# Kernel optimization log

Measured on AMD Instinct MI355X. Metric: run time of the kernel, lower is better.

## Reference

```python
import jax, jax.numpy as jnp
import numpy as np
from jax import lax

DEPTH = 2
HEADS = 8
TEMP = 1.0

def _ln_last(x, g, b, eps=1e-5):
    m = x.mean(-1, keepdims=True)
    v = ((x - m) ** 2).mean(-1, keepdims=True)
    return (x - m) / jnp.sqrt(v + eps) * g + b

def _ln_chan(x, g, b, eps=1e-6):
    # torch custom LayerNorm over channel dim of NCHW, biased var
    m = x.mean(1, keepdims=True)
    v = ((x - m) ** 2).mean(1, keepdims=True)
    return (x - m) / jnp.sqrt(v + eps) * g[None, :, None, None] + b[None, :, None, None]

def _conv3x3(x, w):
    return lax.conv_general_dilated(x, w, (1, 1), ((1, 1), (1, 1)),
                                    dimension_numbers=('NCHW', 'OIHW', 'NCHW'))

def _transformer(x, ln1_g, ln1_b, qkv_w, qkv_b, out_w, out_b, ln2_g, ln2_b,
                 mlp_w1, mlp_b1, mlp_w2, mlp_b2):
    dim = x.shape[-1]
    dh = dim // HEADS
    scale = dh ** -0.5
    for i in range(DEPTH):
        h = _ln_last(x, ln1_g[i], ln1_b[i])
        qkv = h @ qkv_w[i] + qkv_b[i]
        q, k, v = jnp.split(qkv, 3, axis=-1)
        sp = lambda t: t.reshape(t.shape[0], t.shape[1], HEADS, dh).transpose(0, 2, 1, 3)
        q, k, v = sp(q), sp(k), sp(v)
        attn = jax.nn.softmax(jnp.einsum('bhid,bhjd->bhij', q, k) * scale, axis=-1) / TEMP
        o = jnp.einsum('bhij,bhjd->bhid', attn, v).transpose(0, 2, 1, 3).reshape(x.shape)
        x = o @ out_w[i] + out_b[i] + x
        h = _ln_last(x, ln2_g[i], ln2_b[i])
        x = jax.nn.gelu(h @ mlp_w1[i] + mlp_b1[i], approximate=False) @ mlp_w2[i] + mlp_b2[i] + x
    return x

def _tacf(support_feature, query_feature, task_descriptor, ln1_g, ln1_b, qkv_w, qkv_b,
          out_w, out_b, ln2_g, ln2_b, mlp_w1, mlp_b1, mlp_w2, mlp_b2,
          rfm_ln_g, rfm_ln_b, rfm_conv1, rfm_conv2, rfm_conv3, rfm_conv4):
    n, c, h, w = support_feature.shape
    M = task_descriptor.shape[1]
    # descriptor generator: 'n c h w -> 1 (n h w) c', prepend descriptors
    sf = support_feature.transpose(0, 2, 3, 1).reshape(1, n * h * w, c)
    x = jnp.concatenate([task_descriptor, sf], axis=1)
    x = _transformer(x, ln1_g, ln1_b, qkv_w, qkv_b, out_w, out_b, ln2_g, ln2_b,
                     mlp_w1, mlp_b1, mlp_w2, mlp_b2)
    key0 = x[0, :M, :]  # (M, C)

    def region(feat):
        # mean over C of feat[:,None,c,h,w]*key[m,c] == matmul / C
        return jax.nn.sigmoid(jnp.einsum('bchw,mc->bmhw', feat, key0) / feat.shape[1])

    def map_fuse(reg, feat):
        # mean over m of (feat*task + feat) == feat*(mean_m(task)+1)
        return feat * (reg.mean(1, keepdims=True) + 1.0)

    def rfm(x4):
        t = _ln_chan(x4, rfm_ln_g, rfm_ln_b)
        t = jax.nn.relu(_conv3x3(t, rfm_conv1))
        t = jax.nn.relu(_conv3x3(t, rfm_conv2))
        t = jax.nn.relu(_conv3x3(t, rfm_conv3))
        t = _conv3x3(t, rfm_conv4)
        b_, T_, h_, w_ = t.shape
        t = jax.nn.sigmoid(t.reshape(b_, T_, h_ * w_))  # (B,T,HW)
        feat = x4.transpose(0, 2, 3, 1).reshape(b_, h_ * w_, -1)  # (B,HW,C)
        out = jnp.einsum('btp,bpc->btc', t, feat) / (h_ * w_)  # mean over HW
        return out.transpose(0, 2, 1)  # (B,C,T)

    qr = region(query_feature)
    sr = region(support_feature)
    aq = map_fuse(qr, query_feature)
    asp = map_fuse(sr, support_feature)
    return (rfm(asp), rfm(aq))

def setup_inputs() -> dict:
    key = jax.random.key(0)
    ks = jax.random.split(key, 12)
    B_S, B_Q, C, H, W = 25, 75, 128, 10, 10
    M, T, MLP = 16, 32, 512
    rn = lambda k, s, sc=1.0: jax.random.normal(k, s, dtype=jnp.float32) * sc
    return {
        'support_feature': rn(ks[0], (B_S, C, H, W)),
        'query_feature': rn(ks[1], (B_Q, C, H, W)),
        'task_descriptor': rn(ks[2], (1, M, C)),
        'ln1_g': jnp.ones((DEPTH, C), jnp.float32), 'ln1_b': jnp.zeros((DEPTH, C), jnp.float32),
        'qkv_w': rn(ks[3], (DEPTH, C, 3 * C), 0.02), 'qkv_b': jnp.zeros((DEPTH, 3 * C), jnp.float32),
        'out_w': rn(ks[4], (DEPTH, C, C), 0.02), 'out_b': jnp.zeros((DEPTH, C), jnp.float32),
        'ln2_g': jnp.ones((DEPTH, C), jnp.float32), 'ln2_b': jnp.zeros((DEPTH, C), jnp.float32),
        'mlp_w1': rn(ks[5], (DEPTH, C, MLP), 0.02), 'mlp_b1': jnp.zeros((DEPTH, MLP), jnp.float32),
        'mlp_w2': rn(ks[6], (DEPTH, MLP, C), 0.02), 'mlp_b2': jnp.zeros((DEPTH, C), jnp.float32),
        'rfm_ln_g': jnp.ones((C,), jnp.float32), 'rfm_ln_b': jnp.zeros((C,), jnp.float32),
        'rfm_conv1': rn(ks[7], (T, C, 3, 3), 0.05),
        'rfm_conv2': rn(ks[8], (T, T, 3, 3), 0.05),
        'rfm_conv3': rn(ks[9], (T, T, 3, 3), 0.05),
        'rfm_conv4': rn(ks[10], (T, T, 3, 3), 0.05),
    }

def reference(support_feature, query_feature, task_descriptor, ln1_g, ln1_b, qkv_w, qkv_b,
              out_w, out_b, ln2_g, ln2_b, mlp_w1, mlp_b1, mlp_w2, mlp_b2,
              rfm_ln_g, rfm_ln_b, rfm_conv1, rfm_conv2, rfm_conv3, rfm_conv4):
    return _tacf(support_feature, query_feature, task_descriptor, ln1_g, ln1_b, qkv_w, qkv_b,
                 out_w, out_b, ln2_g, ln2_b, mlp_w1, mlp_b1, mlp_w2, mlp_b2,
                 rfm_ln_g, rfm_ln_b, rfm_conv1, rfm_conv2, rfm_conv3, rfm_conv4)
```

## Files before the change

### kernel.cpp

```cpp
#include <hip/hip_runtime.h>
#include <math.h>

#define SEQ 2516
#define SEQP 2520
#define SEQP2 2560
#define CDIM 128

typedef __attribute__((ext_vector_type(8))) short short8;
typedef __attribute__((ext_vector_type(4))) float f32x4;

__device__ __forceinline__ float gelu_exact(float x) {
    return x * 0.5f * (1.0f + erff(x * 0.7071067811865475f));
}
__device__ __forceinline__ float fexp2(float x) { return __builtin_amdgcn_exp2f(x); }
__device__ __forceinline__ short f2bf(float f) {
    unsigned u = __float_as_uint(f);
    unsigned r = 0x7fffu + ((u >> 16) & 1u);
    return (short)((u + r) >> 16);
}
__device__ __forceinline__ short f2bf_trunc(float f) {
    return (short)(__float_as_uint(f) >> 16);
}

__global__ __launch_bounds__(64) void concat_ln_kernel(
// ... 199 lines not shown
    const int grp = __builtin_amdgcn_readfirstlane(t >> 7);
    const int r0 = blockIdx.x * 8 + grp * 2;
    float acc0 = 0.f, acc1 = 0.f;
    #pragma unroll
    for (int h = 0; h < 8; ++h) {
        const float* p0a = PART + ((size_t)h * SEQP + r0) * 20;
        const float* p1a = PART + ((size_t)(8 + h) * SEQP + r0) * 20;
        const float* p0b = p0a + 20;
        const float* p1b = p1a + 20;
        float m0 = p0a[16], l0 = p0a[17], m1 = p1a[16], l1 = p1a[17];
        float Ma = fmaxf(m0, m1);
        float w0 = fexp2(m0 - Ma), w1 = fexp2(m1 - Ma);
        float inva = 1.f / fmaf(l0, w0, l1 * w1);
        float c0a = w0 * inva, c1a = w1 * inva;
        m0 = p0b[16]; l0 = p0b[17]; m1 = p1b[16]; l1 = p1b[17];
        float Mb = fmaxf(m0, m1);
        w0 = fexp2(m0 - Mb); w1 = fexp2(m1 - Mb);
        float invb = 1.f / fmaf(l0, w0, l1 * w1);
        float c0b = w0 * invb, c1b = w1 * invb;
        #pragma unroll
        for (int kk = 0; kk < 4; ++kk) {
            const int k0 = h * 16 + kk * 4;
            float w_0 = W[(size_t)(k0 + 0) * 128 + c];
            float w_1 = W[(size_t)(k0 + 1) * 128 + c];
            float w_2 = W[(size_t)(k0 + 2) * 128 + c];
            float w_3 = W[(size_t)(k0 + 3) * 128 + c];
            float4 x0 = *(const float4*)&p0a[kk * 4];
            float4 y0 = *(const float4*)&p1a[kk * 4];
            float4 x1 = *(const float4*)&p0b[kk * 4];
            float4 y1 = *(const float4*)&p1b[kk * 4];
            float a00 = x0.x * c0a + y0.x * c1a;
            float a01 = x0.y * c0a + y0.y * c1a;
            float a02 = x0.z * c0a + y0.z * c1a;
            float a03 = x0.w * c0a + y0.w * c1a;
            float a10 = x1.x * c0b + y1.x * c1b;
            float a11 = x1.y * c0b + y1.y * c1b;
            float a12 = x1.z * c0b + y1.z * c1b;
            float a13 = x1.w * c0b + y1.w * c1b;
            acc0 = fmaf(a00, w_0, acc0); acc0 = fmaf(a01, w_1, acc0);
            acc0 = fmaf(a02, w_2, acc0); acc0 = fmaf(a03, w_3, acc0);
            acc1 = fmaf(a10, w_0, acc1); acc1 = fmaf(a11, w_1, acc1);
            acc1 = fmaf(a12, w_2, acc1); acc1 = fmaf(a13, w_3, acc1);
        }
    }
    float bv = bias[c];
    float v0 = acc0 + bv + R[(size_t)(r0 + 0) * 128 + c];
    float v1 = acc1 + bv + R[(size_t)(r0 + 1) * 128 + c];
    ln[grp * 2 + 0][c] = v0;
    ln[grp * 2 + 1][c] = v1;
    if (r0 + 0 < M) C[(size_t)(r0 + 0) * 128 + c] = v0;
    if (r0 + 1 < M) C[(size_t)(r0 + 1) * 128 + c] = v1;
    __syncthreads();
    const int wv = t >> 6, l = t & 63;
    float x0 = ln[wv][l], x1 = ln[wv][l + 64];
    float s = x0 + x1;
    for (int off = 32; off > 0; off >>= 1) s += __shfl_down(s, off);
    float mean = __shfl(s, 0) * (1.f / 128.f);
    float d0 = x0 - mean, d1 = x1 - mean;
    float vv = d0 * d0 + d1 * d1;
    for (int off = 32; off > 0; off >>= 1) vv += __shfl_down(vv, off);
    float var = __shfl(vv, 0) * (1.f / 128.f);
    float rstd = rsqrtf(var + 1e-5f);
    const int hrow = blockIdx.x * 8 + wv;
    H[(size_t)hrow * 128 + l]      = d0 * rstd * g[l] + bb[l];
    H[(size_t)hrow * 128 + 64 + l] = d1 * rstd * g[l + 64] + bb[l + 64];
}

__global__ __launch_bounds__(256) void mlp_fused_kernel(
    const float* __restrict__ A, const float* __restrict__ W1,
    const float* __restrict__ b1, const float* __restrict__ W2,
    float* __restrict__ PARTG) {
    __shared__ __align__(16) short W1t[64 * 136];
    __shared__ __align__(16) short W2t[128 * 72];
    __shared__ __align__(16) short Ct[4 * 16 * 72];
    const int t = threadIdx.x;
    const int wave = t >> 6, lane = t & 63;
    const int quad = lane >> 4, c16 = lane & 15;
    const int m0 = blockIdx.x * 64;
    const int kz = blockIdx.y;
    const int n0 = kz * 64;
    #pragma unroll
    for (int pass = 0; pass < 4; ++pass) {
        int idx = t + pass * 256;
        int n = idx & 63, kc = idx >> 6;
        short8 wv;
        #pragma unroll
        for (int j = 0; j < 8; ++j)
            wv[j] = f2bf(W1[(size_t)(kc * 8 + j) * 512 + n0 + n]);
        *(short8*)&W1t[n * 136 + kc * 8] = wv;
    }
    {
        const int n = t & 127, half = t >> 7;
        #pragma unroll
        for (int c = 0; c < 4; ++c) {
            short8 wv;
            #pragma unroll
            for (int j = 0; j < 8; ++j)
                wv[j] = f2bf(W2[(size_t)(n0 + half * 32 + c * 8 + j) * 128 + n]);
            *(short8*)&W2t[n * 72 + half * 32 + c * 8] = wv;
        }
    }
    __syncthreads();
    const int am = m0 + wave * 16 + c16;
    f32x4 acc1[4];
    #pragma unroll
    for (int i = 0; i < 4; ++i) acc1[i] = (f32x4){0.f, 0.f, 0.f, 0.f};
    #pragma unroll
    for (int kk = 0; kk < 4; ++kk) {
        const float4* ap = (const float4*)(A + (size_t)am * 128 + kk * 32 + quad * 8);
        float4 a0 = ap[0], a1 = ap[1];
        short8 af;
        af[0] = f2bf(a0.x); af[1] = f2bf(a0.y); af[2] = f2bf(a0.z); af[3] = f2bf(a0.w);
        af[4] = f2bf(a1.x); af[5] = f2bf(a1.y); af[6] = f2bf(a1.z); af[7] = f2bf(a1.w);
        #pragma unroll
        for (int ns = 0; ns < 4; ++ns) {
            short8 wf = *(const short8*)&W1t[(ns * 16 + c16) * 136 + kk * 32 + quad * 8];
            acc1[ns] = __builtin_amdgcn_mfma_f32_16x16x32_bf16(af, wf, acc1[ns], 0, 0, 0);
        }
    }
    short* Cw = Ct + wave * 16 * 72;
    #pragma unroll
    for (int ns = 0; ns < 4; ++ns) {
        float bv = b1[n0 + ns * 16 + c16];
        #pragma unroll
        for (int r = 0; r < 4; ++r)
            Cw[(quad * 4 + r) * 72 + ns * 16 + c16] = f2bf(gelu_exact(acc1[ns][r] + bv));
    }
    f32x4 acc2[8];
    #pragma unroll
    for (int i = 0; i < 8; ++i) acc2[i] = (f32x4){0.f, 0.f, 0.f, 0.f};
    #pragma unroll
    for (int kk = 0; kk < 2; ++kk) {
        short8 af2 = *(const short8*)&Cw[c16 * 72 + kk * 32 + quad * 8];
        #pragma unroll
        for (int ns = 0; ns < 8; ++ns) {
            short8 wf = *(const short8*)&W2t[(ns * 16 + c16) * 72 + kk * 32 + quad * 8];
            acc2[ns] = __builtin_amdgcn_mfma_f32_16x16x32_bf16(af2, wf, acc2[ns], 0, 0, 0);
        }
    }
    float* dst = PARTG + (size_t)kz * SEQP2 * 128;
    #pragma unroll
    for (int ns = 0; ns < 8; ++ns) {
        #pragma unroll
        for (int r = 0; r < 4; ++r) {
            const int row = m0 + wave * 16 + quad * 4 + r;
            dst[(size_t)row * 128 + ns * 16 + c16] = acc2[ns][r];
        }
    }
}

__global__ __launch_bounds__(512) void combine_ln_kernel(
    const float* __restrict__ PARTG, const float* __restrict__ bias,
    const float* __restrict__ R, float* __restrict__ C, float* __restrict__ H,
    const float* __restrict__ g, const float* __restrict__ bb, int M) {
    __shared__ float ln[8][130];
    const int t = threadIdx.x;
    const int c = t & 127;
    const int grp = __builtin_amdgcn_readfirstlane(t >> 7);
    const int r0 = blockIdx.x * 8 + grp * 2;
    #pragma unroll
    for (int i = 0; i < 2; ++i) {
        const int row = r0 + i;
        float v = bias[c] + R[(size_t)row * 128 + c];
        #pragma unroll
        for (int kz = 0; kz < 8; ++kz)
            v += PARTG[(size_t)kz * SEQP2 * 128 + (size_t)row * 128 + c];
        ln[grp * 2 + i][c] = v;
        if (row < M) C[(size_t)row * 128 + c] = v;
    }
    __syncthreads();
    const int wv = t >> 6, l = t & 63;
    float x0 = ln[wv][l], x1 = ln[wv][l + 64];
    float s = x0 + x1;
    for (int off = 32; off > 0; off >>= 1) s += __shfl_down(s, off);
    float mean = __shfl(s, 0) * (1.f / 128.f);
    float d0 = x0 - mean, d1 = x1 - mean;
    float vv = d0 * d0 + d1 * d1;
    for (int off = 32; off > 0; off >>= 1) vv += __shfl_down(vv, off);
    float var = __shfl(vv, 0) * (1.f / 128.f);
    float rstd = rsqrtf(var + 1e-5f);
    const int hrow = blockIdx.x * 8 + wv;
    H[(size_t)hrow * 128 + l]      = d0 * rstd * g[l] + bb[l];
    H[(size_t)hrow * 128 + 64 + l] = d1 * rstd * g[l + 64] + bb[l + 64];
}

__global__ __launch_bounds__(256) void region_fuse_stats_kernel(
    const float* __restrict__ sup, const float* __restrict__ qry,
    const float* __restrict__ X, float* __restrict__ FUSEDT,
    float* __restrict__ MEAN, float* __restrict__ RSTD) {
    __shared__ float key0[2048];
    __shared__ float rfac[100];
    const int b = blockIdx.x;
    const int t = threadIdx.x;
    const float* feat = (b < 25) ? (sup + (size_t)b * 12800) : (qry + (size_t)(b - 25) * 12800);
    for (int i = t; i < 2048; i += 256) key0[i] = X[i];
    __syncthreads();
    if (t < 100) {
        float dots[16];
        #pragma unroll
        for (int mm = 0; mm < 16; ++mm) dots[mm] = 0.f;
        float s = 0.f, ss = 0.f;
        for (int c = 0; c < 128; ++c) {
            float f = feat[c * 100 + t];
            s += f; ss += f * f;
            #pragma unroll
            for (int mm = 0; mm < 16; ++mm) dots[mm] += f * key0[mm * 128 + c];
        }
        float mean16 = 0.f;
        #pragma unroll
        for (int mm = 0; mm < 16; ++mm) mean16 += 1.f / (1.f + expf(-dots[mm] * (1.f / 128.f)));
        float r = mean16 * (1.f / 16.f) + 1.f;
        rfac[t] = r;
        float mr = s * (1.f / 128.f);
        float vr = ss * (1.f / 128.f) - mr * mr;
        MEAN[b * 128 + t] = mr * r;
        RSTD[b * 128 + t] = rsqrtf(vr * r * r + 1e-6f);
    }
    __syncthreads();
    for (int i = t; i < 12800; i += 256) {
        int p = i >> 7, c = i & 127;
        FUSEDT[(size_t)b * 12800 + i] = feat[c * 100 + p] * rfac[p];
    }
}

__global__ __launch_bounds__(256) void conv1_mfma_kernel(
    const float* __restrict__ FUSEDT, const float* __restrict__ MEAN,
    const float* __restrict__ RSTD, const float* __restrict__ g,
    const float* __restrict__ bb, const float* __restrict__ w,
    short* __restrict__ C1) {
    __shared__ __align__(16) short inT[144 * 136];
    __shared__ __align__(16) short Wt[32 * 136];
    const int b = blockIdx.x;
    const int t = threadIdx.x;
    const int wave = t >> 6, lane = t & 63;
    const int quad = lane >> 4, c16 = lane & 15;
    for (int idx = t; idx < 2304; idx += 256) {
        int pos = idx >> 4, cg = idx & 15;
        int yy = pos / 12, xx = pos - yy * 12;
        short8 sv;
        if (yy >= 1 && yy <= 10 && xx >= 1 && xx <= 10) {
            int pp = (yy - 1) * 10 + (xx - 1);
            const float4* fp = (const float4*)(FUSEDT + (size_t)b * 12800 + pp * 128 + cg * 8);
            float4 f0 = fp[0], f1 = fp[1];
            float mn = MEAN[b * 128 + pp], rs = RSTD[b * 128 + pp];
            float vals[8] = {f0.x, f0.y, f0.z, f0.w, f1.x, f1.y, f1.z, f1.w};
            #pragma unroll
            for (int j = 0; j < 8; ++j)
                sv[j] = f2bf((vals[j] - mn) * rs * g[cg * 8 + j] + bb[cg * 8 + j]);
        } else {
            #pragma unroll
            for (int j = 0; j < 8; ++j) sv[j] = 0;
        }
        *(short8*)&inT[pos * 136 + cg * 8] = sv;
    }
    const int m0 = wave * 32 + c16;
    const int m1 = m0 + 16;
    const int mc0 = (m0 < 100) ? m0 : 99, mc1 = (m1 < 100) ? m1 : 99;
    const int base0 = (mc0 / 10) * 12 + (mc0 % 10);
    const int base1 = (mc1 / 10) * 12 + (mc1 % 10);
    f32x4 a00 = {0.f,0.f,0.f,0.f}, a01 = {0.f,0.f,0.f,0.f};
    f32x4 a10 = {0.f,0.f,0.f,0.f}, a11 = {0.f,0.f,0.f,0.f};
    for (int j = 0; j < 9; ++j) {
        __syncthreads();
        for (int i = t; i < 4096; i += 256) {
            int co = i >> 7, cin = i & 127;
            Wt[co * 136 + cin] = f2bf(w[(size_t)(co * 128 + cin) * 9 + j]);
        }
        __syncthreads();
        const int offj = (j / 3) * 12 + (j % 3);
        #pragma unroll
        for (int kk = 0; kk < 4; ++kk) {
            short8 af0 = *(const short8*)&inT[(base0 + offj) * 136 + kk * 32 + quad * 8];
            short8 af1 = *(const short8*)&inT[(base1 + offj) * 136 + kk * 32 + quad * 8];
            short8 bf0 = *(const short8*)&Wt[c16 * 136 + kk * 32 + quad * 8];
            short8 bf1 = *(const short8*)&Wt[(16 + c16) * 136 + kk * 32 + quad * 8];
            a00 = __builtin_amdgcn_mfma_f32_16x16x32_bf16(af0, bf0, a00, 0, 0, 0);
            a01 = __builtin_amdgcn_mfma_f32_16x16x32_bf16(af0, bf1, a01, 0, 0, 0);
            a10 = __builtin_amdgcn_mfma_f32_16x16x32_bf16(af1, bf0, a10, 0, 0, 0);
            a11 = __builtin_amdgcn_mfma_f32_16x16x32_bf16(af1, bf1, a11, 0, 0, 0);
        }
    }
    #pragma unroll
    for (int r = 0; r < 4; ++r) {
        const int p0 = wave * 32 + quad * 4 + r;
        const int p1 = p0 + 16;
        if (p0 < 100) {
            C1[((size_t)b * 100 + p0) * 32 + c16]      = f2bf(fmaxf(a00[r], 0.f));
            C1[((size_t)b * 100 + p0) * 32 + 16 + c16] = f2bf(fmaxf(a01[r], 0.f));
        }
        if (p1 < 100) {
            C1[((size_t)b * 100 + p1) * 32 + c16]      = f2bf(fmaxf(a10[r], 0.f));
            C1[((size_t)b * 100 + p1) * 32 + 16 + c16] = f2bf(fmaxf(a11[r], 0.f));
        }
    }
}

__global__ __launch_bounds__(256) void conv33_mfma_kernel(
    const short* __restrict__ Cin_, const float* __restrict__ w,
    short* __restrict__ Cout) {
    __shared__ __align__(16) short inT[144 * 40];
    __shared__ __align__(16) short Wt[9 * 32 * 40];
    const int b = blockIdx.x;
    const int t = threadIdx.x;
    const int wave = t >> 6, lane = t & 63;
    const int quad = lane >> 4, c16 = lane & 15;
    for (int i = t; i < 9216; i += 256) {
        int j = i / 1024, rem = i - j * 1024;
        int co = rem >> 5, ch = rem & 31;
        Wt[j * 1280 + co * 40 + ch] = f2bf(w[(size_t)co * 288 + ch * 9 + j]);
    }
    for (int idx = t; idx < 288; idx += 256) {
        int pos = idx >> 1, half = idx & 1;
        int yy = pos / 12, xx = pos - yy * 12;
        short8 s0, s1;
        if (yy >= 1 && yy <= 10 && xx >= 1 && xx <= 10) {
            int pp = (yy - 1) * 10 + (xx - 1);
            const short8* sp = (const short8*)(Cin_ + ((size_t)b * 100 + pp) * 32 + half * 16);
            s0 = sp[0]; s1 = sp[1];
        } else {
            #pragma unroll
            for (int j = 0; j < 8; ++j) { s0[j] = 0; s1[j] = 0; }
        }
        *(short8*)&inT[pos * 40 + half * 16]     = s0;
        *(short8*)&inT[pos * 40 + half * 16 + 8] = s1;
    }
    __syncthreads();
    const int m0 = wave * 32 + c16;
    const int m1 = m0 + 16;
    const int mc0 = (m0 < 100) ? m0 : 99, mc1 = (m1 < 100) ? m1 : 99;
    const int base0 = (mc0 / 10) * 12 + (mc0 % 10);
    const int base1 = (mc1 / 10) * 12 + (mc1 % 10);
    f32x4 a00 = {0.f,0.f,0.f,0.f}, a01 = {0.f,0.f,0.f,0.f};
    f32x4 a10 = {0.f,0.f,0.f,0.f}, a11 = {0.f,0.f,0.f,0.f};
    #pragma unroll
    for (int j = 0; j < 9; ++j) {
        const int offj = (j / 3) * 12 + (j % 3);
        short8 af0 = *(const short8*)&inT[(base0 + offj) * 40 + quad * 8];
        short8 af1 = *(const short8*)&inT[(base1 + offj) * 40 + quad * 8];
        short8 bf0 = *(const short8*)&Wt[j * 1280 + c16 * 40 + quad * 8];
        short8 bf1 = *(const short8*)&Wt[j * 1280 + (16 + c16) * 40 + quad * 8];
        a00 = __builtin_amdgcn_mfma_f32_16x16x32_bf16(af0, bf0, a00, 0, 0, 0);
        a01 = __builtin_amdgcn_mfma_f32_16x16x32_bf16(af0, bf1, a01, 0, 0, 0);
        a10 = __builtin_amdgcn_mfma_f32_16x16x32_bf16(af1, bf0, a10, 0, 0, 0);
        a11 = __builtin_amdgcn_mfma_f32_16x16x32_bf16(af1, bf1, a11, 0, 0, 0);
    }
    #pragma unroll
    for (int r = 0; r < 4; ++r) {
        const int p0 = wave * 32 + quad * 4 + r;
        const int p1 = p0 + 16;
        if (p0 < 100) {
            Cout[((size_t)b * 100 + p0) * 32 + c16]      = f2bf(fmaxf(a00[r], 0.f));
            Cout[((size_t)b * 100 + p0) * 32 + 16 + c16] = f2bf(fmaxf(a01[r], 0.f));
        }
        if (p1 < 100) {
            Cout[((size_t)b * 100 + p1) * 32 + c16]      = f2bf(fmaxf(a10[r], 0.f));
            Cout[((size_t)b * 100 + p1) * 32 + 16 + c16] = f2bf(fmaxf(a11[r], 0.f));
        }
    }
}

__global__ __launch_bounds__(256) void conv4_pool_kernel(
    const short* __restrict__ C3, const float* __restrict__ w,
    const float* __restrict__ FUSEDT, float* __restrict__ out) {
    __shared__ __align__(16) short inT[144 * 40];
    __shared__ __align__(16) short Wt[9 * 32 * 40];
    __shared__ float sig[32 * 104];
    const int b = blockIdx.x;
    const int t = threadIdx.x;
    const int wave = t >> 6, lane = t & 63;
    const int quad = lane >> 4, c16 = lane & 15;
    for (int i = t; i < 9216; i += 256) {
        int j = i / 1024, rem = i - j * 1024;
        int co = rem >> 5, ch = rem & 31;
        Wt[j * 1280 + co * 40 + ch] = f2bf(w[(size_t)co * 288 + ch * 9 + j]);
    }
    for (int idx = t; idx < 288; idx += 256) {
        int pos = idx >> 1, half = idx & 1;
        int yy = pos / 12, xx = pos - yy * 12;
        short8 s0, s1;
        if (yy >= 1 && yy <= 10 && xx >= 1 && xx <= 10) {
            int pp = (yy - 1) * 10 + (xx - 1);
            const short8* sp = (const short8*)(C3 + ((size_t)b * 100 + pp) * 32 + half * 16);
            s0 = sp[0]; s1 = sp[1];
        } else {
            #pragma unroll
            for (int j = 0; j < 8; ++j) { s0[j] = 0; s1[j] = 0; }
        }
        *(short8*)&inT[pos * 40 + half * 16]     = s0;
        *(short8*)&inT[pos * 40 + half * 16 + 8] = s1;
    }
    __syncthreads();
    const int m0 = wave * 32 + c16;
    const int m1 = m0 + 16;
    const int mc0 = (m0 < 100) ? m0 : 99, mc1 = (m1 < 100) ? m1 : 99;
    const int base0 = (mc0 / 10) * 12 + (mc0 % 10);
    const int base1 = (mc1 / 10) * 12 + (mc1 % 10);
    f32x4 a00 = {0.f,0.f,0.f,0.f}, a01 = {0.f,0.f,0.f,0.f};
    f32x4 a10 = {0.f,0.f,0.f,0.f}, a11 = {0.f,0.f,0.f,0.f};
    #pragma unroll
    for (int j = 0; j < 9; ++j) {
        const int offj = (j / 3) * 12 + (j % 3);
        short8 af0 = *(const short8*)&inT[(base0 + offj) * 40 + quad * 8];
        short8 af1 = *(const short8*)&inT[(base1 + offj) * 40 + quad * 8];
        short8 bf0 = *(const short8*)&Wt[j * 1280 + c16 * 40 + quad * 8];
        short8 bf1 = *(const short8*)&Wt[j * 1280 + (16 + c16) * 40 + quad * 8];
        a00 = __builtin_amdgcn_mfma_f32_16x16x32_bf16(af0, bf0, a00, 0, 0, 0);
        a01 = __builtin_amdgcn_mfma_f32_16x16x32_bf16(af0, bf1, a01, 0, 0, 0);
        a10 = __builtin_amdgcn_mfma_f32_16x16x32_bf16(af1, bf0, a10, 0, 0, 0);
        a11 = __builtin_amdgcn_mfma_f32_16x16x32_bf16(af1, bf1, a11, 0, 0, 0);
    }
    #pragma unroll
    for (int r = 0; r < 4; ++r) {
        const int p0 = wave * 32 + quad * 4 + r;
        const int p1 = p0 + 16;
        if (p0 < 100) {
            sig[(c16)      * 104 + p0] = 1.f / (1.f + expf(-a00[r]));
            sig[(16 + c16) * 104 + p0] = 1.f / (1.f + expf(-a01[r]));
        }
        if (p1 < 100) {
            sig[(c16)      * 104 + p1] = 1.f / (1.f + expf(-a10[r]));
            sig[(16 + c16) * 104 + p1] = 1.f / (1.f + expf(-a11[r]));
        }
    }
    __syncthreads();
    const int cc = t & 127, h = t >> 7;
    float accv[16];
    #pragma unroll
    for (int k = 0; k < 16; ++k) accv[k] = 0.f;
    for (int p = 0; p < 100; ++p) {
        float f = FUSEDT[(size_t)b * 12800 + p * 128 + cc];
        #pragma unroll
        for (int k = 0; k < 16; ++k)
            accv[k] = fmaf(sig[(h + 2 * k) * 104 + p], f, accv[k]);
    }
    #pragma unroll
    for (int k = 0; k < 16; ++k)
        out[(size_t)b * 4096 + cc * 32 + (h + 2 * k)] = accv[k] * 0.01f;
}

extern "C" void kernel_launch(void* const* d_in, const int* in_sizes, int n_in,
                              void* d_out, int out_size, void* d_ws, size_t ws_size,
                              hipStream_t stream) {
    (void)in_sizes; (void)n_in; (void)out_size; (void)ws_size;
    const float* sup    = (const float*)d_in[0];
    const float* qry    = (const float*)d_in[1];
    const float* td     = (const float*)d_in[2];
    const float* ln1_g  = (const float*)d_in[3];
    const float* ln1_b  = (const float*)d_in[4];
    const float* qkv_w  = (const float*)d_in[5];
    const float* qkv_b  = (const float*)d_in[6];
    const float* out_w  = (const float*)d_in[7];
    const float* out_b  = (const float*)d_in[8];
    const float* ln2_g  = (const float*)d_in[9];
    const float* ln2_b  = (const float*)d_in[10];
    const float* mlp_w1 = (const float*)d_in[11];
    const float* mlp_b1 = (const float*)d_in[12];
    const float* mlp_w2 = (const float*)d_in[13];
    const float* mlp_b2 = (const float*)d_in[14];
    const float* rg     = (const float*)d_in[15];
    const float* rb     = (const float*)d_in[16];
    const float* c1     = (const float*)d_in[17];
    const float* c2     = (const float*)d_in[18];
    const float* c3     = (const float*)d_in[19];
    const float* c4     = (const float*)d_in[20];
    float* out = (float*)d_out;

    float* ws     = (float*)d_ws;
    float* X      = ws;
    float* H      = X + 327680;
    float* FUSEDT = H + 327680;
    float* MEAN   = FUSEDT + 1280000;
    float* RSTD   = MEAN + 12800;
    short* Qbf    = (short*)(RSTD + 12800);
    short* Kbf    = Qbf + 327680;
    short* VTb    = Kbf + 327680;
    short* C1     = VTb + 327680;
    short* C2     = C1 + 320000;
    short* C3     = C2 + 320000;
    float* PARTG  = (float*)(C3 + 320000);
    float* PART   = PARTG;

    const int SG = (SEQ + 7) / 8;
    const int MT = (SEQ + 63) / 64;

    concat_ln_kernel<<<SEQ, 64, 0, stream>>>(td, sup, ln1_g, ln1_b, X, H);
    for (int i = 0; i < 2; ++i) {
        const int qmt    = (i == 0) ? MT : 1;
        const int atiles = (i == 0) ? (SEQ + 31) / 32 : 1;
        const int sg     = (i == 0) ? SG : 2;
        const int mmt    = (i == 0) ? MT : 1;
        qkv_mfma_kernel<<<dim3(MT, 6), 256, 0, stream>>>(
            H, qkv_w + (size_t)i * 128 * 384, qkv_b + i * 384, Qbf, Kbf, VTb, qmt);
        attn_kernel<<<dim3(atiles, 8, 2), 128, 0, stream>>>(Qbf, Kbf, VTb, PART);
        proj_merge_ln_kernel<<<sg, 512, 0, stream>>>(
            PART, out_w + (size_t)i * 128 * 128, out_b + i * 128, X, X, H,
            ln2_g + i * 128, ln2_b + i * 128, SEQ);
        mlp_fused_kernel<<<dim3(mmt, 8), 256, 0, stream>>>(
            H, mlp_w1 + (size_t)i * 128 * 512, mlp_b1 + i * 512,
            mlp_w2 + (size_t)i * 512 * 128, PARTG);
        const float* ng = (i == 0) ? ln1_g + 128 : ln1_g;
        const float* nb = (i == 0) ? ln1_b + 128 : ln1_b;
        combine_ln_kernel<<<sg, 512, 0, stream>>>(
            PARTG, mlp_b2 + i * 128, X, X, H, ng, nb, SEQ);
    }
    region_fuse_stats_kernel<<<100, 256, 0, stream>>>(sup, qry, X, FUSEDT, MEAN, RSTD);
    conv1_mfma_kernel<<<100, 256, 0, stream>>>(FUSEDT, MEAN, RSTD, rg, rb, c1, C1);
    conv33_mfma_kernel<<<100, 256, 0, stream>>>(C1, c2, C2);
    conv33_mfma_kernel<<<100, 256, 0, stream>>>(C2, c3, C3);
    conv4_pool_kernel<<<100, 256, 0, stream>>>(C3, c4, FUSEDT, out);
}
```

Measured before the change: 274.6 us.

## Fuse second-layer tail, region+conv1, and conv2-4+pool kernels

```diff
diff --git a/kernel.cpp b/kernel.cpp
--- a/kernel.cpp
+++ b/kernel.cpp
@@ -375,9 +375,14 @@
 __global__ __launch_bounds__(512) void combine_ln_kernel(
     const float* __restrict__ PARTG, const float* __restrict__ bias,
     const float* __restrict__ R, float* __restrict__ C, float* __restrict__ H,
-    const float* __restrict__ g, const float* __restrict__ bb, int M) {
+    const float* __restrict__ g, const float* __restrict__ bb, int M,
+    float* __restrict__ zk) {
     __shared__ float ln[8][130];
     const int t = threadIdx.x;
+    if (zk != nullptr && blockIdx.x == 0) {
+        #pragma unroll
+        for (int i = 0; i < 4; ++i) zk[t + i * 512] = 0.f;
+    }
     const int c = t & 127;
     const int grp = __builtin_amdgcn_readfirstlane(t >> 7);
     const int r0 = blockIdx.x * 8 + grp * 2;
@@ -407,74 +412,204 @@
     H[(size_t)hrow * 128 + 64 + l] = d1 * rstd * g[l + 64] + bb[l + 64];
 }
 
-__global__ __launch_bounds__(256) void region_fuse_stats_kernel(
+__global__ __launch_bounds__(512) void pml16_kernel(
+    const float* __restrict__ PART, const float* __restrict__ Wo,
+    const float* __restrict__ ob, const float* __restrict__ g2,
+    const float* __restrict__ bl2, const float* __restrict__ W1,
+    const float* __restrict__ b1, const float* __restrict__ W2,
+    const float* __restrict__ b2, const float* __restrict__ X,
+    float* __restrict__ KEY0) {
+    __shared__ __align__(16) char SMEM[4352 + 38912];
+    short* hA   = (short*)SMEM;
+    char*  U    = SMEM + 4352;
+    float* PARTL = (float*)U;
+    float* coefL = PARTL + 5120;
+    float* xpL   = coefL + 256;
+    short* W1t  = (short*)U;
+    short* W2t  = W1t + 8704;
+    short* Ct   = W2t + 9216;
+    const int t = threadIdx.x;
+    const int kz = blockIdx.x;
+
+    for (int i = t; i < 5120; i += 512) {
+        int sh = i / 320, rem = i - sh * 320;
+        PARTL[i] = PART[((size_t)sh * SEQP) * 20 + rem];
+    }
+    __syncthreads();
+    if (t < 128) {
+        int row = t >> 3, h = t & 7;
+        float ma = PARTL[h * 320 + row * 20 + 16];
+        float la = PARTL[h * 320 + row * 20 + 17];
+        float mb = PARTL[(8 + h) * 320 + row * 20 + 16];
+        float lb = PARTL[(8 + h) * 320 + row * 20 + 17];
+        float Mx = fmaxf(ma, mb);
+        float w0 = fexp2(ma - Mx), w1 = fexp2(mb - Mx);
+        float inv = 1.f / fmaf(la, w0, lb * w1);
+        coefL[row * 16 + h * 2]     = w0 * inv;
+        coefL[row * 16 + h * 2 + 1] = w1 * inv;
+    }
+    __syncthreads();
+    const int c = t & 127;
+    const int grp = t >> 7;
+    float xv[4] = {0.f, 0.f, 0.f, 0.f};
+    for (int h = 0; h < 8; ++h) {
+        float c0v[4], c1v[4];
+        #pragma unroll
+        for (int i = 0; i < 4; ++i) {
+            int row = grp * 4 + i;
+            c0v[i] = coefL[row * 16 + h * 2];
+            c1v[i] = coefL[row * 16 + h * 2 + 1];
+        }
+        #pragma unroll
+        for (int d = 0; d < 16; ++d) {
+            float w = Wo[(size_t)(h * 16 + d) * 128 + c];
+            #pragma unroll
+            for (int i = 0; i < 4; ++i) {
+                int row = grp * 4 + i;
+                float a = PARTL[h * 320 + row * 20 + d] * c0v[i]
+                        + PARTL[(8 + h) * 320 + row * 20 + d] * c1v[i];
+                xv[i] = fmaf(a, w, xv[i]);
+            }
+        }
+    }
+    #pragma unroll
+    for (int i = 0; i < 4; ++i) {
+        int row = grp * 4 + i;
+        float v = xv[i] + ob[c] + X[(size_t)row * 128 + c];
+        xpL[row * 130 + c] = v;
+        if (kz == 0) atomicAdd(&KEY0[row * 128 + c], v + b2[c]);
+    }
+    __syncthreads();
+    {
+        const int wv6 = t >> 6, l = t & 63;
+        #pragma unroll
+        for (int rr = 0; rr < 2; ++rr) {
+            int row = wv6 * 2 + rr;
+            float x0 = xpL[row * 130 + l], x1 = xpL[row * 130 + 64 + l];
+            float s = x0 + x1;
+            s += __shfl_xor(s, 1); s += __shfl_xor(s, 2); s += __shfl_xor(s, 4);
+            s += __shfl_xor(s, 8); s += __shfl_xor(s, 16); s += __shfl_xor(s, 32);
+            float mean = s * (1.f / 128.f);
+            float d0 = x0 - mean, d1 = x1 - mean;
+            float vv = d0 * d0 + d1 * d1;
+            vv += __shfl_xor(vv, 1); vv += __shfl_xor(vv, 2); vv += __shfl_xor(vv, 4);
+            vv += __shfl_xor(vv, 8); vv += __shfl_xor(vv, 16); vv += __shfl_xor(vv, 32);
+            float rstd = rsqrtf(vv * (1.f / 128.f) + 1e-5f);
+            hA[row * 136 + l]      = f2bf(d0 * rstd * g2[l] + bl2[l]);
+            hA[row * 136 + 64 + l] = f2bf(d1 * rstd * g2[64 + l] + bl2[64 + l]);
+        }
+    }
+    __syncthreads();
+    for (int idx = t; idx < 1024; idx += 512) {
+        int n = idx & 63, kc = idx >> 6;
+        short8 wv;
+        #pragma unroll
+        for (int j = 0; j < 8; ++j)
+            wv[j] = f2bf(W1[(size_t)(kc * 8 + j) * 512 + kz * 64 + n]);
+        *(short8*)&W1t[n * 136 + kc * 8] = wv;
+    }
+    for (int idx = t; idx < 1024; idx += 512) {
+        int n = idx & 127, kc = idx >> 7;
+        short8 wv;
+        #pragma unroll
+        for (int j = 0; j < 8; ++j)
+            wv[j] = f2bf(W2[(size_t)(kz * 64 + kc * 8 + j) * 128 + n]);
+        *(short8*)&W2t[n * 72 + kc * 8] = wv;
+    }
+    __syncthreads();
+    if (t < 64) {
+        const int quad = t >> 4, c16 = t & 15;
+        f32x4 acc1[4];
+        #pragma unroll
+        for (int i = 0; i < 4; ++i) acc1[i] = (f32x4){0.f, 0.f, 0.f, 0.f};
+        #pragma unroll
+        for (int kk = 0; kk < 4; ++kk) {
+            short8 af = *(const short8*)&hA[c16 * 136 + kk * 32 + quad * 8];
+            #pragma unroll
+            for (int ns = 0; ns < 4; ++ns) {
+                short8 wf = *(const short8*)&W1t[(ns * 16 + c16) * 136 + kk * 32 + quad * 8];
+                acc1[ns] = __builtin_amdgcn_mfma_f32_16x16x32_bf16(af, wf, acc1[ns], 0, 0, 0);
+            }
+        }
+        #pragma unroll
+        for (int ns = 0; ns < 4; ++ns) {
+            float bv = b1[kz * 64 + ns * 16 + c16];
+            #pragma unroll
+            for (int r = 0; r < 4; ++r)
+                Ct[(quad * 4 + r) * 72 + ns * 16 + c16] = f2bf(gelu_exact(acc1[ns][r] + bv));
+        }
+        f32x4 acc2[8];
+        #pragma unroll
+        for (int i = 0; i < 8; ++i) acc2[i] = (f32x4){0.f, 0.f, 0.f, 0.f};
+        #pragma unroll
+        for (int kk = 0; kk < 2; ++kk) {
+            short8 af2 = *(const short8*)&Ct[c16 * 72 + kk * 32 + quad * 8];
+            #pragma unroll
+            for (int ns = 0; ns < 8; ++ns) {
+                short8 wf = *(const short8*)&W2t[(ns * 16 + c16) * 72 + kk * 32 + quad * 8];
+                acc2[ns] = __builtin_amdgcn_mfma_f32_16x16x32_bf16(af2, wf, acc2[ns], 0, 0, 0);
+            }
+        }
+        #pragma unroll
+        for (int ns = 0; ns < 8; ++ns) {
+            #pragma unroll
+            for (int r = 0; r < 4; ++r)
+                atomicAdd(&KEY0[(quad * 4 + r) * 128 + ns * 16 + c16], acc2[ns][r]);
+        }
+    }
+}
+
+__global__ __launch_bounds__(256) void region_conv1_kernel(
     const float* __restrict__ sup, const float* __restrict__ qry,
-    const float* __restrict__ X, float* __restrict__ FUSEDT,
-    float* __restrict__ MEAN, float* __restrict__ RSTD) {
-    __shared__ float key0[2048];
-    __shared__ float rfac[100];
-    const int b = blockIdx.x;
-    const int t = threadIdx.x;
-    const float* feat = (b < 25) ? (sup + (size_t)b * 12800) : (qry + (size_t)(b - 25) * 12800);
-    for (int i = t; i < 2048; i += 256) key0[i] = X[i];
-    __syncthreads();
-    if (t < 100) {
-        float dots[16];
-        #pragma unroll
-        for (int mm = 0; mm < 16; ++mm) dots[mm] = 0.f;
-        float s = 0.f, ss = 0.f;
-        for (int c = 0; c < 128; ++c) {
-            float f = feat[c * 100 + t];
-            s += f; ss += f * f;
-            #pragma unroll
-            for (int mm = 0; mm < 16; ++mm) dots[mm] += f * key0[mm * 128 + c];
-        }
-        float mean16 = 0.f;
-        #pragma unroll
-        for (int mm = 0; mm < 16; ++mm) mean16 += 1.f / (1.f + expf(-dots[mm] * (1.f / 128.f)));
-        float r = mean16 * (1.f / 16.f) + 1.f;
-        rfac[t] = r;
-        float mr = s * (1.f / 128.f);
-        float vr = ss * (1.f / 128.f) - mr * mr;
-        MEAN[b * 128 + t] = mr * r;
-        RSTD[b * 128 + t] = rsqrtf(vr * r * r + 1e-6f);
-    }
-    __syncthreads();
-    for (int i = t; i < 12800; i += 256) {
-        int p = i >> 7, c = i & 127;
-        FUSEDT[(size_t)b * 12800 + i] = feat[c * 100 + p] * rfac[p];
-    }
-}
-
-__global__ __launch_bounds__(256) void conv1_mfma_kernel(
-    const float* __restrict__ FUSEDT, const float* __restrict__ MEAN,
-    const float* __restrict__ RSTD, const float* __restrict__ g,
-    const float* __restrict__ bb, const float* __restrict__ w,
-    short* __restrict__ C1) {
+    const float* __restrict__ KEY0, const float* __restrict__ rg,
+    const float* __restrict__ rb, const float* __restrict__ w,
+    short* __restrict__ C1, float* __restrict__ RFAC) {
+    __shared__ float key0L[2048];
+    __shared__ float rfacL[104], MEANL[104], RSTDL[104];
     __shared__ __align__(16) short inT[144 * 136];
     __shared__ __align__(16) short Wt[32 * 136];
     const int b = blockIdx.x;
     const int t = threadIdx.x;
     const int wave = t >> 6, lane = t & 63;
     const int quad = lane >> 4, c16 = lane & 15;
-    for (int idx = t; idx < 2304; idx += 256) {
-        int pos = idx >> 4, cg = idx & 15;
-        int yy = pos / 12, xx = pos - yy * 12;
-        short8 sv;
-        if (yy >= 1 && yy <= 10 && xx >= 1 && xx <= 10) {
-            int pp = (yy - 1) * 10 + (xx - 1);
-            const float4* fp = (const float4*)(FUSEDT + (size_t)b * 12800 + pp * 128 + cg * 8);
-            float4 f0 = fp[0], f1 = fp[1];
-            float mn = MEAN[b * 128 + pp], rs = RSTD[b * 128 + pp];
-            float vals[8] = {f0.x, f0.y, f0.z, f0.w, f1.x, f1.y, f1.z, f1.w};
-            #pragma unroll
-            for (int j = 0; j < 8; ++j)
-                sv[j] = f2bf((vals[j] - mn) * rs * g[cg * 8 + j] + bb[cg * 8 + j]);
-        } else {
-            #pragma unroll
-            for (int j = 0; j < 8; ++j) sv[j] = 0;
-        }
-        *(short8*)&inT[pos * 136 + cg * 8] = sv;
+    const float* feat = (b < 25) ? (sup + (size_t)b * 12800) : (qry + (size_t)(b - 25) * 12800);
+    for (int i = t; i < 2048; i += 256) key0L[i] = KEY0[i];
+    for (int i = t; i < 2448; i += 256) {
+        short8 z; 
+        #pragma unroll
+        for (int j = 0; j < 8; ++j) z[j] = 0;
+        *(short8*)&inT[i * 8] = z;
+    }
+    __syncthreads();
+    if (t < 100) {
+        float dots[16];
+        #pragma unroll
+        for (int mm = 0; mm < 16; ++mm) dots[mm] = 0.f;
+        float s = 0.f, ss = 0.f;
+        for (int c = 0; c < 128; ++c) {
+            float f = feat[c * 100 + t];
+            s += f; ss = fmaf(f, f, ss);
+            #pragma unroll
+            for (int mm = 0; mm < 16; ++mm) dots[mm] = fmaf(f, key0L[mm * 128 + c], dots[mm]);
+        }
+        float m16 = 0.f;
+        #pragma unroll
+        for (int mm = 0; mm < 16; ++mm) m16 += 1.f / (1.f + expf(-dots[mm] * (1.f / 128.f)));
+        float r = m16 * (1.f / 16.f) + 1.f;
+        rfacL[t] = r;
+        RFAC[b * 100 + t] = r;
+        float mr = s * (1.f / 128.f);
+        float vr = ss * (1.f / 128.f) - mr * mr;
+        MEANL[t] = mr * r;
+        RSTDL[t] = rsqrtf(vr * r * r + 1e-6f);
+    }
+    __syncthreads();
+    for (int i = t; i < 12800; i += 256) {
+        int cc = i / 100, p = i - cc * 100;
+        float v = feat[i] * rfacL[p];
+        float lnv = (v - MEANL[p]) * RSTDL[p] * rg[cc] + rb[cc];
+        int pos = (p / 10 + 1) * 12 + (p % 10) + 1;
+        inT[pos * 136 + cc] = f2bf(lnv);
     }
     const int m0 = wave * 32 + c16;
     const int m1 = m0 + 16;
@@ -518,131 +653,107 @@
     }
 }
 
-__global__ __launch_bounds__(256) void conv33_mfma_kernel(
-    const short* __restrict__ Cin_, const float* __restrict__ w,
-    short* __restrict__ Cout) {
-    __shared__ __align__(16) short inT[144 * 40];
+__global__ __launch_bounds__(256) void conv234_pool_kernel(
+    const short* __restrict__ C1, const float* __restrict__ w2,
+    const float* __restrict__ w3, const float* __restrict__ w4,
+    const float* __restrict__ sup, const float* __restrict__ qry,
+    const float* __restrict__ RFAC, float* __restrict__ out) {
+    __shared__ __align__(16) short inTA[144 * 40];
+    __shared__ __align__(16) short inTB[144 * 40];
     __shared__ __align__(16) short Wt[9 * 32 * 40];
+    __shared__ float sig[32 * 104];
+    __shared__ float rfacL[104];
     const int b = blockIdx.x;
     const int t = threadIdx.x;
     const int wave = t >> 6, lane = t & 63;
     const int quad = lane >> 4, c16 = lane & 15;
-    for (int i = t; i < 9216; i += 256) {
-        int j = i / 1024, rem = i - j * 1024;
-        int co = rem >> 5, ch = rem & 31;
-        Wt[j * 1280 + co * 40 + ch] = f2bf(w[(size_t)co * 288 + ch * 9 + j]);
-    }
-    for (int idx = t; idx < 288; idx += 256) {
-        int pos = idx >> 1, half = idx & 1;
-        int yy = pos / 12, xx = pos - yy * 12;
-        short8 s0, s1;
-        if (yy >= 1 && yy <= 10 && xx >= 1 && xx <= 10) {
-            int pp = (yy - 1) * 10 + (xx - 1);
-            const short8* sp = (const short8*)(Cin_ + ((size_t)b * 100 + pp) * 32 + half * 16);
-            s0 = sp[0]; s1 = sp[1];
-        } else {
-            #pragma unroll
-            for (int j = 0; j < 8; ++j) { s0[j] = 0; s1[j] = 0; }
-        }
-        *(short8*)&inT[pos * 40 + half * 16]     = s0;
-        *(short8*)&inT[pos * 40 + half * 16 + 8] = s1;
-    }
-    __syncthreads();
+    const float* feat = (b < 25) ? (sup + (size_t)b * 12800) : (qry + (size_t)(b - 25) * 12800);
+    for (int i = t; i < 720; i += 256) {
+        short8 z;
+        #pragma unroll
+        for (int j = 0; j < 8; ++j) z[j] = 0;
+        *(short8*)&inTA[i * 8] = z;
+        *(short8*)&inTB[i * 8] = z;
+    }
+    if (t < 100) rfacL[t] = RFAC[b * 100 + t];
+    __syncthreads();
+    for (int idx = t; idx < 200; idx += 256) {
+        int pp = idx >> 1, half = idx & 1;
+        int pos = (pp / 10 + 1) * 12 + (pp % 10) + 1;
+        const short8* sp = (const short8*)(C1 + ((size_t)b * 100 + pp) * 32 + half * 16);
+        *(short8*)&inTA[pos * 40 + half * 16]     = sp[0];
+        *(short8*)&inTA[pos * 40 + half * 16 + 8] = sp[1];
+    }
     const int m0 = wave * 32 + c16;
     const int m1 = m0 + 16;
     const int mc0 = (m0 < 100) ? m0 : 99, mc1 = (m1 < 100) ? m1 : 99;
     const int base0 = (mc0 / 10) * 12 + (mc0 % 10);
     const int base1 = (mc1 / 10) * 12 + (mc1 % 10);
-    f32x4 a00 = {0.f,0.f,0.f,0.f}, a01 = {0.f,0.f,0.f,0.f};
-    f32x4 a10 = {0.f,0.f,0.f,0.f}, a11 = {0.f,0.f,0.f,0.f};
-    #pragma unroll
-    for (int j = 0; j < 9; ++j) {
-        const int offj = (j / 3) * 12 + (j % 3);
-        short8 af0 = *(const short8*)&inT[(base0 + offj) * 40 + quad * 8];
-        short8 af1 = *(const short8*)&inT[(base1 + offj) * 40 + quad * 8];
-        short8 bf0 = *(const short8*)&Wt[j * 1280 + c16 * 40 + quad * 8];
-        short8 bf1 = *(const short8*)&Wt[j * 1280 + (16 + c16) * 40 + quad * 8];
-        a00 = __builtin_amdgcn_mfma_f32_16x16x32_bf16(af0, bf0, a00, 0, 0, 0);
-        a01 = __builtin_amdgcn_mfma_f32_16x16x32_bf16(af0, bf1, a01, 0, 0, 0);
-        a10 = __builtin_amdgcn_mfma_f32_16x16x32_bf16(af1, bf0, a10, 0, 0, 0);
-        a11 = __builtin_amdgcn_mfma_f32_16x16x32_bf16(af1, bf1, a11, 0, 0, 0);
-    }
+    const int p0o = wave * 32 + quad * 4;
+    f32x4 a00, a01, a10, a11;
+
+#define STAGE_W(wptr)                                                        \
+    for (int i = t; i < 9216; i += 256) {                                    \
+        int j = i / 1024, rem = i - j * 1024;                                \
+        int co = rem >> 5, ch = rem & 31;                                    \
+        Wt[j * 1280 + co * 40 + ch] = f2bf((wptr)[(size_t)co * 288 + ch * 9 + j]); \
+    }
+#define CONV(src)                                                            \
+    a00 = (f32x4){0.f,0.f,0.f,0.f}; a01 = (f32x4){0.f,0.f,0.f,0.f};          \
+    a10 = (f32x4){0.f,0.f,0.f,0.f}; a11 = (f32x4){0.f,0.f,0.f,0.f};          \
+    _Pragma("unroll")                                                        \
+    for (int j = 0; j < 9; ++j) {                                            \
+        const int offj = (j / 3) * 12 + (j % 3);                             \
+        short8 af0 = *(const short8*)&(src)[(base0 + offj) * 40 + quad * 8]; \
+        short8 af1 = *(const short8*)&(src)[(base1 + offj) * 40 + quad * 8]; \
+        short8 bf0 = *(const short8*)&Wt[j * 1280 + c16 * 40 + quad * 8];    \
+        short8 bf1 = *(const short8*)&Wt[j * 1280 + (16 + c16) * 40 + quad * 8]; \
+        a00 = __builtin_amdgcn_mfma_f32_16x16x32_bf16(af0, bf0, a00, 0, 0, 0); \
+        a01 = __builtin_amdgcn_mfma_f32_16x16x32_bf16(af0, bf1, a01, 0, 0, 0); \
+        a10 = __builtin_amdgcn_mfma_f32_16x16x32_bf16(af1, bf0, a10, 0, 0, 0); \
+        a11 = __builtin_amdgcn_mfma_f32_16x16x32_bf16(af1, bf1, a11, 0, 0, 0); \
+    }
+#define WRITE_RELU(dst)                                                      \
+    _Pragma("unroll")                                                        \
+    for (int r = 0; r < 4; ++r) {                                            \
+        const int q0 = p0o + r, q1 = q0 + 16;                                \
+        if (q0 < 100) {                                                      \
+            int ps = (q0 / 10 + 1) * 12 + (q0 % 10) + 1;                     \
+            (dst)[ps * 40 + c16]      = f2bf(fmaxf(a00[r], 0.f));            \
+            (dst)[ps * 40 + 16 + c16] = f2bf(fmaxf(a01[r], 0.f));            \
+        }                                                                    \
+        if (q1 < 100) {                                                      \
+            int ps = (q1 / 10 + 1) * 12 + (q1 % 10) + 1;                     \
+            (dst)[ps * 40 + c16]      = f2bf(fmaxf(a10[r], 0.f));            \
+            (dst)[ps * 40 + 16 + c16] = f2bf(fmaxf(a11[r], 0.f));            \
+        }                                                                    \
+    }
+
+    STAGE_W(w2)
+    __syncthreads();
+    CONV(inTA)
+    __syncthreads();
+    WRITE_RELU(inTB)
+    STAGE_W(w3)
+    __syncthreads();
+    CONV(inTB)
+    __syncthreads();
+    WRITE_RELU(inTA)
+    STAGE_W(w4)
+    __syncthreads();
+    CONV(inTA)
     #pragma unroll
     for (int r = 0; r < 4; ++r) {
-        const int p0 = wave * 32 + quad * 4 + r;
-        const int p1 = p0 + 16;
-        if (p0 < 100) {
-            Cout[((size_t)b * 100 + p0) * 32 + c16]      = f2bf(fmaxf(a00[r], 0.f));
-            Cout[((size_t)b * 100 + p0) * 32 + 16 + c16] = f2bf(fmaxf(a01[r], 0.f));
-        }
-        if (p1 < 100) {
-            Cout[((size_t)b * 100 + p1) * 32 + c16]      = f2bf(fmaxf(a10[r], 0.f));
-            Cout[((size_t)b * 100 + p1) * 32 + 16 + c16] = f2bf(fmaxf(a11[r], 0.f));
-        }
-    }
-}
-
-__global__ __launch_bounds__(256) void conv4_pool_kernel(
-    const short* __restrict__ C3, const float* __restrict__ w,
-    const float* __restrict__ FUSEDT, float* __restrict__ out) {
-    __shared__ __align__(16) short inT[144 * 40];
-    __shared__ __align__(16) short Wt[9 * 32 * 40];
-    __shared__ float sig[32 * 104];
-    const int b = blockIdx.x;
-    const int t = threadIdx.x;
-    const int wave = t >> 6, lane = t & 63;
-    const int quad = lane >> 4, c16 = lane & 15;
-    for (int i = t; i < 9216; i += 256) {
-        int j = i / 1024, rem = i - j * 1024;
-        int co = rem >> 5, ch = rem & 31;
-        Wt[j * 1280 + co * 40 + ch] = f2bf(w[(size_t)co * 288 + ch * 9 + j]);
-    }
-    for (int idx = t; idx < 288; idx += 256) {
-        int pos = idx >> 1, half = idx & 1;
-        int yy = pos / 12, xx = pos - yy * 12;
-        short8 s0, s1;
-        if (yy >= 1 && yy <= 10 && xx >= 1 && xx <= 10) {
-            int pp = (yy - 1) * 10 + (xx - 1);
-            const short8* sp = (const short8*)(C3 + ((size_t)b * 100 + pp) * 32 + half * 16);
-            s0 = sp[0]; s1 = sp[1];
-        } else {
-            #pragma unroll
-            for (int j = 0; j < 8; ++j) { s0[j] = 0; s1[j] = 0; }
-        }
-        *(short8*)&inT[pos * 40 + half * 16]     = s0;
-        *(short8*)&inT[pos * 40 + half * 16 + 8] = s1;
-    }
-    __syncthreads();
-    const int m0 = wave * 32 + c16;
-    const int m1 = m0 + 16;
-    const int mc0 = (m0 < 100) ? m0 : 99, mc1 = (m1 < 100) ? m1 : 99;
-    const int base0 = (mc0 / 10) * 12 + (mc0 % 10);
-    const int base1 = (mc1 / 10) * 12 + (mc1 % 10);
-    f32x4 a00 = {0.f,0.f,0.f,0.f}, a01 = {0.f,0.f,0.f,0.f};
-    f32x4 a10 = {0.f,0.f,0.f,0.f}, a11 = {0.f,0.f,0.f,0.f};
-    #pragma unroll
-    for (int j = 0; j < 9; ++j) {
-        const int offj = (j / 3) * 12 + (j % 3);
-        short8 af0 = *(const short8*)&inT[(base0 + offj) * 40 + quad * 8];
-        short8 af1 = *(const short8*)&inT[(base1 + offj) * 40 + quad * 8];
-        short8 bf0 = *(const short8*)&Wt[j * 1280 + c16 * 40 + quad * 8];
-        short8 bf1 = *(const short8*)&Wt[j * 1280 + (16 + c16) * 40 + quad * 8];
-        a00 = __builtin_amdgcn_mfma_f32_16x16x32_bf16(af0, bf0, a00, 0, 0, 0);
-        a01 = __builtin_amdgcn_mfma_f32_16x16x32_bf16(af0, bf1, a01, 0, 0, 0);
-        a10 = __builtin_amdgcn_mfma_f32_16x16x32_bf16(af1, bf0, a10, 0, 0, 0);
-        a11 = __builtin_amdgcn_mfma_f32_16x16x32_bf16(af1, bf1, a11, 0, 0, 0);
-    }
-    #pragma unroll
-    for (int r = 0; r < 4; ++r) {
-        const int p0 = wave * 32 + quad * 4 + r;
-        const int p1 = p0 + 16;
-        if (p0 < 100) {
-            sig[(c16)      * 104 + p0] = 1.f / (1.f + expf(-a00[r]));
-            sig[(16 + c16) * 104 + p0] = 1.f / (1.f + expf(-a01[r]));
-        }
-        if (p1 < 100) {
-            sig[(c16)      * 104 + p1] = 1.f / (1.f + expf(-a10[r]));
-            sig[(16 + c16) * 104 + p1] = 1.f / (1.f + expf(-a11[r]));
+        const int q0 = p0o + r, q1 = q0 + 16;
+        if (q0 < 100) {
+            float rf = rfacL[q0];
+            sig[c16 * 104 + q0]        = rf / (1.f + expf(-a00[r]));
+            sig[(16 + c16) * 104 + q0] = rf / (1.f + expf(-a01[r]));
+        }
+        if (q1 < 100) {
+            float rf = rfacL[q1];
+            sig[c16 * 104 + q1]        = rf / (1.f + expf(-a10[r]));
+            sig[(16 + c16) * 104 + q1] = rf / (1.f + expf(-a11[r]));
         }
     }
     __syncthreads();
@@ -650,15 +761,21 @@
     float accv[16];
     #pragma unroll
     for (int k = 0; k < 16; ++k) accv[k] = 0.f;
-    for (int p = 0; p < 100; ++p) {
-        float f = FUSEDT[(size_t)b * 12800 + p * 128 + cc];
-        #pragma unroll
-        for (int k = 0; k < 16; ++k)
-            accv[k] = fmaf(sig[(h + 2 * k) * 104 + p], f, accv[k]);
+    const float* fp = feat + (size_t)cc * 100;
+    for (int pp = 0; pp < 100; pp += 4) {
+        float4 f4 = *(const float4*)&fp[pp];
+        #pragma unroll
+        for (int k = 0; k < 16; ++k) {
+            const float* sg = &sig[(h + 2 * k) * 104 + pp];
+            accv[k] += sg[0] * f4.x + sg[1] * f4.y + sg[2] * f4.z + sg[3] * f4.w;
+        }
     }
     #pragma unroll
     for (int k = 0; k < 16; ++k)
         out[(size_t)b * 4096 + cc * 32 + (h + 2 * k)] = accv[k] * 0.01f;
+#undef STAGE_W
+#undef CONV
+#undef WRITE_RELU
 }
 
 extern "C" void kernel_launch(void* const* d_in, const int* in_sizes, int n_in,
@@ -688,47 +805,38 @@
     const float* c4     = (const float*)d_in[20];
     float* out = (float*)d_out;
 
-    float* ws     = (float*)d_ws;
-    float* X      = ws;
-    float* H      = X + 327680;
-    float* FUSEDT = H + 327680;
-    float* MEAN   = FUSEDT + 1280000;
-    float* RSTD   = MEAN + 12800;
-    short* Qbf    = (short*)(RSTD + 12800);
-    short* Kbf    = Qbf + 327680;
-    short* VTb    = Kbf + 327680;
-    short* C1     = VTb + 327680;
-    short* C2     = C1 + 320000;
-    short* C3     = C2 + 320000;
-    float* PARTG  = (float*)(C3 + 320000);
-    float* PART   = PARTG;
+    float* ws    = (float*)d_ws;
+    float* X     = ws;
+    float* H     = X + 327680;
+    float* KEY0  = H + 327680;
+    float* RFAC  = KEY0 + 2048;
+    short* Qbf   = (short*)(RFAC + 10000);
+    short* Kbf   = Qbf + 327680;
+    short* VTb   = Kbf + 327680;
+    short* C1    = VTb + 327680;
+    float* PARTG = (float*)(C1 + 320000);
+    float* PART  = PARTG;
 
     const int SG = (SEQ + 7) / 8;
     const int MT = (SEQ + 63) / 64;
 
     concat_ln_kernel<<<SEQ, 64, 0, stream>>>(td, sup, ln1_g, ln1_b, X, H);
-    for (int i = 0; i < 2; ++i) {
-        const int qmt    = (i == 0) ? MT : 1;
-        const int atiles = (i == 0) ? (SEQ + 31) / 32 : 1;
-        const int sg     = (i == 0) ? SG : 2;
-        const int mmt    = (i == 0) ? MT : 1;
-        qkv_mfma_kernel<<<dim3(MT, 6), 256, 0, stream>>>(
-            H, qkv_w + (size_t)i * 128 * 384, qkv_b + i * 384, Qbf, Kbf, VTb, qmt);
-        attn_kernel<<<dim3(atiles, 8, 2), 128, 0, stream>>>(Qbf, Kbf, VTb, PART);
-        proj_merge_ln_kernel<<<sg, 512, 0, stream>>>(
-            PART, out_w + (size_t)i * 128 * 128, out_b + i * 128, X, X, H,
-            ln2_g + i * 128, ln2_b + i * 128, SEQ);
-        mlp_fused_kernel<<<dim3(mmt, 8), 256, 0, stream>>>(
-            H, mlp_w1 + (size_t)i * 128 * 512, mlp_b1 + i * 512,
-            mlp_w2 + (size_t)i * 512 * 128, PARTG);
-        const float* ng = (i == 0) ? ln1_g + 128 : ln1_g;
-        const float* nb = (i == 0) ? ln1_b + 128 : ln1_b;
-        combine_ln_kernel<<<sg, 512, 0, stream>>>(
-            PARTG, mlp_b2 + i * 128, X, X, H, ng, nb, SEQ);
-    }
-    region_fuse_stats_kernel<<<100, 256, 0, stream>>>(sup, qry, X, FUSEDT, MEAN, RSTD);
-    conv1_mfma_kernel<<<100, 256, 0, stream>>>(FUSEDT, MEAN, RSTD, rg, rb, c1, C1);
-    conv33_mfma_kernel<<<100, 256, 0, stream>>>(C1, c2, C2);
-    conv33_mfma_kernel<<<100, 256, 0, stream>>>(C2, c3, C3);
-    conv4_pool_kernel<<<100, 256, 0, stream>>>(C3, c4, FUSEDT, out);
-}
+    qkv_mfma_kernel<<<dim3(MT, 6), 256, 0, stream>>>(
+        H, qkv_w, qkv_b, Qbf, Kbf, VTb, MT);
+    attn_kernel<<<dim3((SEQ + 31) / 32, 8, 2), 128, 0, stream>>>(Qbf, Kbf, VTb, PART);
+    proj_merge_ln_kernel<<<SG, 512, 0, stream>>>(
+        PART, out_w, out_b, X, X, H, ln2_g, ln2_b, SEQ);
+    mlp_fused_kernel<<<dim3(MT, 8), 256, 0, stream>>>(
+        H, mlp_w1, mlp_b1, mlp_w2, PARTG);
+    combine_ln_kernel<<<SG, 512, 0, stream>>>(
+        PARTG, mlp_b2, X, X, H, ln1_g + 128, ln1_b + 128, SEQ, KEY0);
+    qkv_mfma_kernel<<<dim3(MT, 6), 256, 0, stream>>>(
+        H, qkv_w + (size_t)128 * 384, qkv_b + 384, Qbf, Kbf, VTb, 1);
+    attn_kernel<<<dim3(1, 8, 2), 128, 0, stream>>>(Qbf, Kbf, VTb, PART);
+    pml16_kernel<<<8, 512, 0, stream>>>(
+        PART, out_w + 128 * 128, out_b + 128, ln2_g + 128, ln2_b + 128,
+        mlp_w1 + (size_t)128 * 512, mlp_b1 + 512, mlp_w2 + (size_t)512 * 128,
+        mlp_b2 + 128, X, KEY0);
+    region_conv1_kernel<<<100, 256, 0, stream>>>(sup, qry, KEY0, rg, rb, c1, C1, RFAC);
+    conv234_pool_kernel<<<100, 256, 0, stream>>>(C1, c2, c3, c4, sup, qry, RFAC, out);
+}
```

Result: faster. 262.6 us (-4.4%).
